# Kernel optimization log

Hardware: AMD Instinct MI355X
Metric: run time of the kernel (lower is better)

## Reference

```python
import jax, jax.numpy as jnp
import numpy as np

# Config: 2 base samples x 3 views, 128x128 feature map, d_model=128, 8x8 window grid
D = 128; H = 128; W = 128; NS = 8; NV = 3; BV = 2
B = BV * NV            # batched views (queries concatenated along batch)
M = NV - 1             # kv views per query view
WH = H // NS; WW = W // NS; WSZ = WH * WW
SH = WH // 2; SW = WW // 2  # shift sizes


def _split_np(f, ns):  # channel-last split_feature, numpy (for mask gen)
    b, h, w, c = f.shape
    return f.reshape(b, ns, h // ns, ns, w // ns, c).transpose(0, 1, 3, 2, 4, 5).reshape(b * ns * ns, h // ns, w // ns, c)


def _make_mask():  # generate_shift_window_attn_mask, structurally identical
    img = np.zeros((1, H, W, 1), np.float32)
    h_sl = [(0, H - WH), (H - WH, H - SH), (H - SH, H)]
    w_sl = [(0, W - WW), (W - WW, W - SW), (W - SW, W)]
    cnt = 0
    for h0, h1 in h_sl:
        for w0, w1 in w_sl:
            img[:, h0:h1, w0:w1, :] = cnt
            cnt += 1
    mw = _split_np(img, NS).reshape(-1, WSZ)               # [num_windows, WSZ]
    am = mw[:, None, :] - mw[:, :, None]
    return np.where(am != 0, np.float32(-100.0), np.float32(0.0))


def setup_inputs() -> dict:
    key = jax.random.key(0)
    ks = jax.random.split(key, 12)
    s = 1.0 / np.sqrt(D)
    s2 = 1.0 / np.sqrt(2 * D)
    s8 = 1.0 / np.sqrt(8 * D)
    f32 = jnp.float32
    inp = {
        'source': jax.random.normal(ks[0], (B, H * W, D), f32),
        'kv': jax.random.normal(ks[1], (B, M, H * W, D), f32),
        'attn_mask': jnp.asarray(_make_mask()),
        # self-attn layer (no ffn)
        'q1_w': jax.random.normal(ks[2], (D, D), f32) * s,
        'k1_w': jax.random.normal(ks[3], (D, D), f32) * s,
        'v1_w': jax.random.normal(ks[4], (D, D), f32) * s,
        'merge1_w': jax.random.normal(ks[5], (D, D), f32) * s,
        'ln1_g': jnp.ones((D,), f32), 'ln1_b': jnp.zeros((D,), f32),
        # cross-attn + ffn layer
        'q2_w': jax.random.normal(ks[6], (D, D), f32) * s,
        'k2_w': jax.random.normal(ks[7], (D, D), f32) * s,
        'v2_w': jax.random.normal(ks[8], (D, D), f32) * s,
        'merge2_w': jax.random.normal(ks[9], (D, D), f32) * s,
        'ln2a_g': jnp.ones((D,), f32), 'ln2a_b': jnp.zeros((D,), f32),
        'mlp_w1': jax.random.normal(ks[10], (2 * D, 8 * D), f32) * s2,
        'mlp_w2': jax.random.normal(ks[11], (8 * D, D), f32) * s8,
        'ln2b_g': jnp.ones((D,), f32), 'ln2b_b': jnp.zeros((D,), f32),
        'height': H, 'width': W, 'num_splits': NS,
    }
    return inp


def _split(x, ns):  # channel-last split_feature
    b, h, w, c = x.shape
    return x.reshape(b, ns, h // ns, ns, w // ns, c).transpose(0, 1, 3, 2, 4, 5).reshape(b * ns * ns, h // ns, w // ns, c)


def _merge(x, ns):  # channel-last merge_splits
    b, h, w, c = x.shape
    nb = b // (ns * ns)
    return x.reshape(nb, ns, ns, h, w, c).transpose(0, 1, 3, 2, 4, 5).reshape(nb, ns * h, ns * w, c)


def _ln(x, g, b):
    mu = x.mean(-1, keepdims=True)
    v = ((x - mu) ** 2).mean(-1, keepdims=True)
    return (x - mu) / jnp.sqrt(v + 1e-5) * g + b


def _self_win_attn(q, k, v, mask, h, w, ns):  # 3-dim path, with_shift=True
    b, _, c = q.shape
    sh, sw = (h // ns) // 2, (w // ns) // 2
    q = jnp.roll(q.reshape(b, h, w, c), (-sh, -sw), (1, 2))
    k = jnp.roll(k.reshape(b, h, w, c), (-sh, -sw), (1, 2))
    v = jnp.roll(v.reshape(b, h, w, c), (-sh, -sw), (1, 2))
    bn = b * ns * ns
    qf = _split(q, ns).reshape(bn, -1, c)
    kf = _split(k, ns).reshape(bn, -1, c)
    vf = _split(v, ns).reshape(bn, -1, c)
    sc = jnp.einsum('bqc,bkc->bqk', qf, kf) / (c ** 0.5) + jnp.tile(mask, (b, 1, 1))
    out = jax.nn.softmax(sc, -1) @ vf
    out = _merge(out.reshape(bn, h // ns, w // ns, c), ns)
    out = jnp.roll(out, (sh, sw), (1, 2))
    return out.reshape(b, -1, c)


def _cross_win_attn(q, k, v, mask, h, w, ns):  # 4-dim path (multi-view kv), with_shift=True
    b, _, c = q.shape
    m = k.shape[1]
    sh, sw = (h // ns) // 2, (w // ns) // 2
    q = jnp.roll(q.reshape(b, h, w, c), (-sh, -sw), (1, 2))
    k = jnp.roll(k.reshape(b, m, h, w, c), (-sh, -sw), (2, 3))
    v = jnp.roll(v.reshape(b, m, h, w, c), (-sh, -sw), (2, 3))
    bn = b * ns * ns
    wh, ww = h // ns, w // ns
    qf = _split(q, ns).reshape(bn, -1, c)
    kf = _split(jnp.transpose(k, (0, 2, 3, 4, 1)).reshape(b, h, w, c * m), ns)
    vf = _split(jnp.transpose(v, (0, 2, 3, 4, 1)).reshape(b, h, w, c * m), ns)
    kmat = jnp.transpose(kf.reshape(bn, wh, ww, c, m), (0, 3, 1, 2, 4)).reshape(bn, c, -1)  # [bn,c,WSZ*m]
    vmat = jnp.transpose(vf.reshape(bn, wh, ww, c, m), (0, 1, 2, 4, 3)).reshape(bn, -1, c)  # [bn,WSZ*m,c]
    sc = jnp.einsum('bqc,bck->bqk', qf, kmat) / (c ** 0.5) + jnp.tile(mask, (b, 1, m))
    out = jax.nn.softmax(sc, -1) @ vmat
    out = _merge(out.reshape(bn, wh, ww, c), ns)
    out = jnp.roll(out, (sh, sw), (1, 2))
    return out.reshape(b, -1, c)


def reference(source, kv, attn_mask, q1_w, k1_w, v1_w, merge1_w, ln1_g, ln1_b,
              q2_w, k2_w, v2_w, merge2_w, ln2a_g, ln2a_b, mlp_w1, mlp_w2, ln2b_g, ln2b_b,
              height, width, num_splits):
    h, w, ns = int(height), int(width), int(num_splits)
    # self-attention TransformerLayer (no_ffn=True)
    msg = _self_win_attn(source @ q1_w, source @ k1_w, source @ v1_w, attn_mask, h, w, ns)
    msg = _ln(msg @ merge1_w, ln1_g, ln1_b)
    src = source + msg
    # cross-attention TransformerLayer with FFN
    msg = _cross_win_attn(src @ q2_w, kv @ k2_w, kv @ v2_w, attn_mask, h, w, ns)
    msg = _ln(msg @ merge2_w, ln2a_g, ln2a_b)
    hid = jnp.concatenate([src, msg], -1) @ mlp_w1
    msg = _ln(jax.nn.gelu(hid, approximate=False) @ mlp_w2, ln2b_g, ln2b_b)
    return src + msg
```

## Files before the change

kernel.cpp:

```cpp
#include <hip/hip_runtime.h>
#include <math.h>


typedef float f4 __attribute__((ext_vector_type(4)));
typedef float f2 __attribute__((ext_vector_type(2)));
typedef float f32x4 __attribute__((ext_vector_type(4)));
typedef short s16x8 __attribute__((ext_vector_type(8)));
typedef short s16x4 __attribute__((ext_vector_type(4)));
typedef unsigned short u16;

constexpr int Dm   = 128;
constexpr int IH   = 128, IW = 128;
constexpr int Bq   = 6;
constexpr int Mv   = 2;
constexpr int WSZ  = 256;
constexpr int TOK  = IH * IW;
constexpr int ROWS = Bq * TOK;
constexpr int KVROWS = Bq * Mv * TOK;
constexpr int BN   = Bq * 64;
constexpr float SCALE = 0.08838834764831845f;

__device__ __forceinline__ u16 f2bf(float x) {
  union { float f; unsigned u; } v; v.f = x;
  unsigned r = v.u + 0x7fffu + ((v.u >> 16) & 1u);
  return (u16)(r >> 16);
}
__device__ __forceinline__ float bf2f(u16 h) {
  union { float f; unsigned u; } v; v.u = ((unsigned)h) << 16;
  return v.f;
}

__device__ __forceinline__ int dest_row_self(int r) {
  int b = r >> 14;
  int p = r & 16383;
  int y = p >> 7, x = p & 127;
  int Y = (y + 120) & 127, X = (x + 120) & 127;
  int bn = (b << 6) + ((Y >> 4) << 3) + (X >> 4);
  int t  = ((Y & 15) << 4) + (X & 15);
  return bn * WSZ + t;
}

__device__ __forceinline__ int dest_row_cross(int r) {
  int b  = r >> 15;
  int vi = (r >> 14) & 1;
  int p  = r & 16383;
  int y = p >> 7, x = p & 127;
  int Y = (y + 120) & 127, X = (x + 120) & 127;
  int bn = (b << 6) + ((Y >> 4) << 3) + (X >> 4);
  int t  = ((Y & 15) << 4) + (X & 15);
  return bn * (WSZ * Mv) + t * Mv + vi;
}

template<int NMAT, int MODE>
__global__ __launch_bounds__(256, 2)
void proj_kernel(const float* __restrict__ A,
                 const float* __restrict__ B0, const float* __restrict__ B1,
                 const float* __restrict__ B2,
                 float* __restrict__ O0, float* __restrict__ O1,
                 float* __restrict__ O2)
{
  __shared__ float At[128][68];
  __shared__ float Bs[64][132];
  const int tid  = threadIdx.x;
  const int row0 = blockIdx.x * 64;

  {
    const int tr = tid >> 2;
    const int tc = (tid & 3) * 4;
    const float* Ar = A + (size_t)(row0 + tr) * Dm;
    #pragma unroll
    for (int i = 0; i < 8; ++i) {
      int c = tc + i * 16;
      f4 a = *(const f4*)(Ar + c);
      At[c + 0][tr] = a[0];
      At[c + 1][tr] = a[1];
      At[c + 2][tr] = a[2];
      At[c + 3][tr] = a[3];
    }
  }

  const int tcol = tid & 31;
  const int trow = tid >> 5;

  int drow[8];
  #pragma unroll
  for (int i = 0; i < 8; ++i) {
    int r = row0 + trow * 8 + i;
    drow[i] = (MODE == 2) ? dest_row_cross(r) : dest_row_self(r);
  }

  #pragma unroll
  for (int m = 0; m < NMAT; ++m) {
    const float* Bm = (m == 0) ? B0 : ((m == 1) ? B1 : B2);
    float*       Om = (m == 0) ? O0 : ((m == 1) ? O1 : O2);
    float acc[8][4];
    #pragma unroll
    for (int i = 0; i < 8; ++i)
      #pragma unroll
      for (int j = 0; j < 4; ++j) acc[i][j] = 0.f;

    for (int kc = 0; kc < 2; ++kc) {
      __syncthreads();
      {
        int kb = tid >> 2;
        int cb = (tid & 3) * 4;
        #pragma unroll
        for (int i = 0; i < 8; ++i) {
          int c = cb + i * 16;
          f4 b = *(const f4*)(Bm + (size_t)(kc * 64 + kb) * Dm + c);
          *(f4*)&Bs[kb][c] = b;
        }
      }
      __syncthreads();
      #pragma unroll 4
      for (int k = 0; k < 64; ++k) {
        int kg = kc * 64 + k;
        f4 a0 = *(const f4*)&At[kg][trow * 8];
        f4 a1 = *(const f4*)&At[kg][trow * 8 + 4];
        f4 b  = *(const f4*)&Bs[k][tcol * 4];
        #pragma unroll
        for (int j = 0; j < 4; ++j) {
          acc[0][j] += a0[0] * b[j];
          acc[1][j] += a0[1] * b[j];
          acc[2][j] += a0[2] * b[j];
          acc[3][j] += a0[3] * b[j];
          acc[4][j] += a1[0] * b[j];
          acc[5][j] += a1[1] * b[j];
          acc[6][j] += a1[2] * b[j];
          acc[7][j] += a1[3] * b[j];
        }
      }
    }
    #pragma unroll
    for (int i = 0; i < 8; ++i) {
      f4 o;
      o[0] = acc[i][0]; o[1] = acc[i][1]; o[2] = acc[i][2]; o[3] = acc[i][3];
      *(f4*)(Om + (size_t)drow[i] * Dm + tcol * 4) = o;
    }
  }
}

template<int MM>
__global__ __launch_bounds__(512, 2)
void attn_kernel(const float* __restrict__ Qw, const float* __restrict__ Kw,
                 const float* __restrict__ Vw, float* __restrict__ X)
{
  constexpr int KC = WSZ * MM;
  __shared__ float Qt[128][36];
  __shared__ float Stg[128 * 132];
  __shared__ float S[32][KC + 1];

  const int tid = threadIdx.x;
  const int bn  = blockIdx.y;
  const int q0  = blockIdx.x * 32;
  const int b   = bn >> 6;
  const int win = bn & 63;
  const int wy  = win >> 3, wx = win & 7;

  {
    const float* Qbase = Qw + ((size_t)bn * WSZ + q0) * Dm;
    #pragma unroll
    for (int j = 0; j < 2; ++j) {
      int id  = tid + j * 512;
      int row = id >> 5;
      int c   = (id & 31) * 4;
      f4 a = *(const f4*)(Qbase + row * Dm + c);
      Qt[c + 0][row] = a[0]; Qt[c + 1][row] = a[1];
      Qt[c + 2][row] = a[2]; Qt[c + 3][row] = a[3];
    }
  }

  auto region = [&](int t) -> int {
    int rh = (wy == 7) ? (((t >> 4) >= 8) ? 2 : 1) : 0;
    int rw = (wx == 7) ? (((t & 15) >= 8) ? 2 : 1) : 0;
    return rh * 3 + rw;
  };

  const int kg = tid & 31;
  const int qg = tid >> 5;
  const int rq0 = region(q0 + qg * 2);
  const int rq1 = region(q0 + qg * 2 + 1);

  for (int ch = 0; ch < KC / 128; ++ch) {
    __syncthreads();
    #pragma unroll
    for (int j = 0; j < 8; ++j) {
      int id  = tid + j * 512;
      int key = id >> 5;
      int c   = (id & 31) * 4;
      f4 kvv = *(const f4*)(Kw + ((size_t)bn * KC + ch * 128 + key) * Dm + c);
      Stg[(c + 0) * 132 + key] = kvv[0];
      Stg[(c + 1) * 132 + key] = kvv[1];
      Stg[(c + 2) * 132 + key] = kvv[2];
      Stg[(c + 3) * 132 + key] = kvv[3];
    }
    __syncthreads();
    float a00 = 0, a01 = 0, a02 = 0, a03 = 0;
    float a10 = 0, a11 = 0, a12 = 0, a13 = 0;
    #pragma unroll 4
    for (int c = 0; c < 128; ++c) {
      f2 qv  = *(const f2*)&Qt[c][qg * 2];
      f4 kv4 = *(const f4*)&Stg[c * 132 + kg * 4];
      a00 += qv[0] * kv4[0]; a01 += qv[0] * kv4[1];
      a02 += qv[0] * kv4[2]; a03 += qv[0] * kv4[3];
      a10 += qv[1] * kv4[0]; a11 += qv[1] * kv4[1];
      a12 += qv[1] * kv4[2]; a13 += qv[1] * kv4[3];
    }
    float s0[4] = {a00, a01, a02, a03};
    float s1[4] = {a10, a11, a12, a13};
    #pragma unroll
    for (int j = 0; j < 4; ++j) {
      int kk = ch * 128 + kg * 4 + j;
      int rk = region(kk & 255);
      S[qg * 2 + 0][kk] = s0[j] * SCALE + ((rq0 == rk) ? 0.f : -100.f);
      S[qg * 2 + 1][kk] = s1[j] * SCALE + ((rq1 == rk) ? 0.f : -100.f);
    }
  }
  __syncthreads();

  {
    int row = tid >> 4, l = tid & 15;
    float mx = -1e30f;
    for (int k = l; k < KC; k += 16) mx = fmaxf(mx, S[row][k]);
    #pragma unroll
    for (int msk = 1; msk < 16; msk <<= 1) mx = fmaxf(mx, __shfl_xor(mx, msk));
    float sum = 0.f;
    for (int k = l; k < KC; k += 16) {
      float e = expf(S[row][k] - mx);
      S[row][k] = e;
      sum += e;
    }
    #pragma unroll
    for (int msk = 1; msk < 16; msk <<= 1) sum += __shfl_xor(sum, msk);
    float inv = 1.0f / sum;
    for (int k = l; k < KC; k += 16) S[row][k] *= inv;
  }

  const int cg = tid & 31;
  const int rg = tid >> 5;
  float o00 = 0, o01 = 0, o02 = 0, o03 = 0;
  float o10 = 0, o11 = 0, o12 = 0, o13 = 0;
  for (int ch = 0; ch < KC / 128; ++ch) {
    __syncthreads();
    #pragma unroll
    for (int j = 0; j < 8; ++j) {
      int id  = tid + j * 512;
      int key = id >> 5;
      int c   = (id & 31) * 4;
      f4 vv = *(const f4*)(Vw + ((size_t)bn * KC + ch * 128 + key) * Dm + c);
      *(f4*)&Stg[key * 132 + c] = vv;
    }
    __syncthreads();
    #pragma unroll 4
    for (int k = 0; k < 128; ++k) {
      int kk = ch * 128 + k;
      float p0 = S[rg * 2 + 0][kk];
      float p1 = S[rg * 2 + 1][kk];
      f4 vv = *(const f4*)&Stg[k * 132 + cg * 4];
      o00 += p0 * vv[0]; o01 += p0 * vv[1]; o02 += p0 * vv[2]; o03 += p0 * vv[3];
      o10 += p1 * vv[0]; o11 += p1 * vv[1]; o12 += p1 * vv[2]; o13 += p1 * vv[3];
    }
  }
  #pragma unroll
  for (int i = 0; i < 2; ++i) {
    int t  = q0 + rg * 2 + i;
    int iy = t >> 4, ix = t & 15;
    int y = (wy * 16 + iy + 8) & 127;
    int x = (wx * 16 + ix + 8) & 127;
    f4 o;
    if (i == 0) { o[0] = o00; o[1] = o01; o[2] = o02; o[3] = o03; }
    else        { o[0] = o10; o[1] = o11; o[2] = o12; o[3] = o13; }
    *(f4*)(X + ((size_t)(b * TOK + y * IW + x)) * Dm + cg * 4) = o;
  }
}

template<bool ADD>
__global__ __launch_bounds__(256, 2)
void merge_ln_kernel(const float* __restrict__ Xin, const float* __restrict__ Wm,
                     const float* __restrict__ g, const float* __restrict__ bi,
                     const float* __restrict__ srcAdd, float* __restrict__ Out)
{
  __shared__ float At[128][68];
  __shared__ float Bs[64][132];
  const int tid  = threadIdx.x;
  const int row0 = blockIdx.x * 64;

  {
    const int tr = tid >> 2;
    const int tc = (tid & 3) * 4;
    const float* Ar = Xin + (size_t)(row0 + tr) * Dm;
    #pragma unroll
    for (int i = 0; i < 8; ++i) {
      int c = tc + i * 16;
      f4 a = *(const f4*)(Ar + c);
      At[c + 0][tr] = a[0]; At[c + 1][tr] = a[1];
      At[c + 2][tr] = a[2]; At[c + 3][tr] = a[3];
    }
  }

  const int tcol = tid & 31;
  const int trow = tid >> 5;
  float acc[8][4];
  #pragma unroll
  for (int i = 0; i < 8; ++i)
    #pragma unroll
    for (int j = 0; j < 4; ++j) acc[i][j] = 0.f;

  for (int kc = 0; kc < 2; ++kc) {
    __syncthreads();
    {
      int kb = tid >> 2;
      int cb = (tid & 3) * 4;
      #pragma unroll
      for (int i = 0; i < 8; ++i) {
        int c = cb + i * 16;
        f4 b = *(const f4*)(Wm + (size_t)(kc * 64 + kb) * Dm + c);
        *(f4*)&Bs[kb][c] = b;
      }
    }
    __syncthreads();
    #pragma unroll 4
    for (int k = 0; k < 64; ++k) {
      int kg = kc * 64 + k;
      f4 a0 = *(const f4*)&At[kg][trow * 8];
      f4 a1 = *(const f4*)&At[kg][trow * 8 + 4];
      f4 b  = *(const f4*)&Bs[k][tcol * 4];
      #pragma unroll
      for (int j = 0; j < 4; ++j) {
        acc[0][j] += a0[0] * b[j];
        acc[1][j] += a0[1] * b[j];
        acc[2][j] += a0[2] * b[j];
        acc[3][j] += a0[3] * b[j];
        acc[4][j] += a1[0] * b[j];
        acc[5][j] += a1[1] * b[j];
        acc[6][j] += a1[2] * b[j];
        acc[7][j] += a1[3] * b[j];
      }
    }
  }

  f4 g4 = *(const f4*)(g + tcol * 4);
  f4 b4 = *(const f4*)(bi + tcol * 4);
  #pragma unroll
  for (int i = 0; i < 8; ++i) {
    float s = acc[i][0] + acc[i][1] + acc[i][2] + acc[i][3];
    #pragma unroll
    for (int msk = 1; msk < 32; msk <<= 1) s += __shfl_xor(s, msk);
    float mu = s * (1.0f / 128.0f);
    float d0 = acc[i][0] - mu, d1 = acc[i][1] - mu;
    float d2 = acc[i][2] - mu, d3 = acc[i][3] - mu;
    float qs = d0 * d0 + d1 * d1 + d2 * d2 + d3 * d3;
    #pragma unroll
    for (int msk = 1; msk < 32; msk <<= 1) qs += __shfl_xor(qs, msk);
    float rstd = 1.0f / sqrtf(qs * (1.0f / 128.0f) + 1e-5f);
    int r = row0 + trow * 8 + i;
    f4 o;
    o[0] = d0 * rstd * g4[0] + b4[0];
    o[1] = d1 * rstd * g4[1] + b4[1];
    o[2] = d2 * rstd * g4[2] + b4[2];
    o[3] = d3 * rstd * g4[3] + b4[3];
    if (ADD) {
      f4 sv = *(const f4*)(srcAdd + (size_t)r * Dm + tcol * 4);
      o += sv;
    }
    *(f4*)(Out + (size_t)r * Dm + tcol * 4) = o;
  }
}

__global__ __launch_bounds__(256)
void prep_weights(const float* __restrict__ W1, const float* __restrict__ W2,
                  u16* __restrict__ w1h, u16* __restrict__ w1l,
                  u16* __restrict__ w2h, u16* __restrict__ w2l)
{
  int id = blockIdx.x * 256 + threadIdx.x;
  if (id < 262144) {
    int i  = id & 7;
    int ln = (id >> 3) & 63;
    int ks = (id >> 9) & 7;
    int ct = (id >> 12) & 7;
    int c  = id >> 15;
    int k   = ks * 32 + (ln >> 4) * 8 + i;
    int col = c * 128 + ct * 16 + (ln & 15);
    float v = W1[(size_t)k * 1024 + col];
    u16 h = f2bf(v);
    w1h[id] = h;
    w1l[id] = f2bf(v - bf2f(h));
  } else {
    int id2 = id - 262144;
    int i  = id2 & 7;
    int ln = (id2 >> 3) & 63;
    int ct = (id2 >> 9) & 7;
    int ks = (id2 >> 12) & 3;
    int c  = id2 >> 14;
    int k   = c * 128 + ks * 32 + (ln >> 4) * 8 + i;
    int col = ct * 16 + (ln & 15);
    float v = W2[(size_t)k * 128 + col];
    u16 h = f2bf(v);
    w2h[id2] = h;
    w2l[id2] = f2bf(v - bf2f(h));
  }
}

__global__ __launch_bounds__(512)
void mlp_mfma_kernel(const float* __restrict__ SRC, const float* __restrict__ MSG,
                     const u16* __restrict__ w1h, const u16* __restrict__ w1l,
                     const u16* __restrict__ w2h, const u16* __restrict__ w2l,
                     const float* __restrict__ g, const float* __restrict__ bi,
                     float* __restrict__ Out)
{
  __shared__ __align__(16) u16 Xh[64 * 256];
  __shared__ __align__(16) u16 Xl[64 * 256];
  __shared__ __align__(16) u16 Hh[64 * 128];
  __shared__ __align__(16) u16 Hl[64 * 128];

  const int tid  = threadIdx.x;
  const int row0 = blockIdx.x * 64;
  const int l    = tid & 63;
  const int w    = tid >> 6;
  const int rt   = w & 3;
  const int ctg  = w >> 2;

  #pragma unroll
  for (int s = 0; s < 8; ++s) {
    int slot = tid + s * 512;
    int row  = slot >> 6;
    int c4   = (slot & 63) * 4;
    const float* p = (c4 < 128) ? (SRC + (size_t)(row0 + row) * Dm + c4)
                                : (MSG + (size_t)(row0 + row) * Dm + (c4 - 128));
    f4 a = *(const f4*)p;
    s16x4 hv, lv;
    #pragma unroll
    for (int i = 0; i < 4; ++i) {
// ... 110 lines not shown
      int cc = sub * 4 + s * 32;
      f4 g4 = *(const f4*)(g + cc);
      f4 b4 = *(const f4*)(bi + cc);
      f4 rv = *(const f4*)(SRC + (size_t)(row0 + row) * Dm + cc);
      f4 o = v[s] * rstd * g4 + b4 + rv;
      *(f4*)(Out + (size_t)(row0 + row) * Dm + cc) = o;
    }
  }
}

extern "C" void kernel_launch(void* const* d_in, const int* in_sizes, int n_in,
                              void* d_out, int out_size, void* d_ws, size_t ws_size,
                              hipStream_t stream)
{
  const float* source = (const float*)d_in[0];
  const float* kv     = (const float*)d_in[1];
  const float* q1    = (const float*)d_in[3];
  const float* k1    = (const float*)d_in[4];
  const float* v1    = (const float*)d_in[5];
  const float* m1    = (const float*)d_in[6];
  const float* ln1g  = (const float*)d_in[7];
  const float* ln1b  = (const float*)d_in[8];
  const float* q2    = (const float*)d_in[9];
  const float* k2    = (const float*)d_in[10];
  const float* v2    = (const float*)d_in[11];
  const float* m2    = (const float*)d_in[12];
  const float* ln2ag = (const float*)d_in[13];
  const float* ln2ab = (const float*)d_in[14];
  const float* w1    = (const float*)d_in[15];
  const float* w2    = (const float*)d_in[16];
  const float* ln2bg = (const float*)d_in[17];
  const float* ln2bb = (const float*)d_in[18];

  float* ws   = (float*)d_ws;
  float* Qw   = ws;
  float* Kw   = Qw + (size_t)BN * WSZ * Dm;
  float* Vw   = Kw + (size_t)BN * WSZ * Mv * Dm;
  float* SRCb = Vw + (size_t)BN * WSZ * Mv * Dm;
  float* MSG2 = Qw;
  float* X    = (float*)d_out;

  u16* w1h = (u16*)Vw;
  u16* w1l = w1h + 262144;
  u16* w2h = w1l + 262144;
  u16* w2l = w2h + 131072;

  proj_kernel<3, 0><<<ROWS / 64, 256, 0, stream>>>(source, q1, k1, v1, Qw, Kw, Vw);
  attn_kernel<1><<<dim3(8, BN), 512, 0, stream>>>(Qw, Kw, Vw, X);
  merge_ln_kernel<true><<<ROWS / 64, 256, 0, stream>>>(X, m1, ln1g, ln1b, source, SRCb);
  proj_kernel<1, 1><<<ROWS / 64, 256, 0, stream>>>(SRCb, q2, nullptr, nullptr,
                                                   Qw, nullptr, nullptr);
  proj_kernel<2, 2><<<KVROWS / 64, 256, 0, stream>>>(kv, k2, v2, nullptr,
                                                     Kw, Vw, nullptr);
  attn_kernel<2><<<dim3(8, BN), 512, 0, stream>>>(Qw, Kw, Vw, X);
  merge_ln_kernel<false><<<ROWS / 64, 256, 0, stream>>>(X, m2, ln2ag, ln2ab,
                                                        nullptr, MSG2);
  prep_weights<<<1536, 256, 0, stream>>>(w1, w2, w1h, w1l, w2h, w2l);
  mlp_mfma_kernel<<<ROWS / 64, 512, 0, stream>>>(SRCb, MSG2, w1h, w1l, w2h, w2l,
                                                 ln2bg, ln2bb, (float*)d_out);
}
```

Baseline: 2.455 ms.

## Move projections, window attention and merge to split-bf16 MFMA kernels

Replaces the scalar fp32 projection, attention and merge+LayerNorm kernels with MFMA versions that split each operand into bf16 high/low parts (three products per tile) to stay close to fp32 accuracy. Attention becomes a flash-style online softmax over 64-key chunks with a transposed V layout, and projections gather rows from window order rather than scattering outputs. Weight fragments are prepared by small prep kernels, and the workspace buffers are laid out again to hold the hi/lo arrays. The aim is to move the dominant FLOPs onto matrix cores, at the cost of triple MFMA work and more intermediate memory traffic for the hi/lo bf16 copies.

```diff
diff --git a/kernel.cpp b/kernel.cpp
--- a/kernel.cpp
+++ b/kernel.cpp
@@ -3,20 +3,17 @@
 
 
 typedef float f4 __attribute__((ext_vector_type(4)));
-typedef float f2 __attribute__((ext_vector_type(2)));
 typedef float f32x4 __attribute__((ext_vector_type(4)));
 typedef short s16x8 __attribute__((ext_vector_type(8)));
 typedef short s16x4 __attribute__((ext_vector_type(4)));
 typedef unsigned short u16;
 
 constexpr int Dm   = 128;
-constexpr int IH   = 128, IW = 128;
 constexpr int Bq   = 6;
 constexpr int Mv   = 2;
 constexpr int WSZ  = 256;
-constexpr int TOK  = IH * IW;
+constexpr int TOK  = 16384;
 constexpr int ROWS = Bq * TOK;
-constexpr int KVROWS = Bq * Mv * TOK;
 constexpr int BN   = Bq * 64;
 constexpr float SCALE = 0.08838834764831845f;
 
@@ -30,374 +27,463 @@
   return v.f;
 }
 
-__device__ __forceinline__ int dest_row_self(int r) {
-  int b = r >> 14;
-  int p = r & 16383;
-  int y = p >> 7, x = p & 127;
-  int Y = (y + 120) & 127, X = (x + 120) & 127;
-  int bn = (b << 6) + ((Y >> 4) << 3) + (X >> 4);
-  int t  = ((Y & 15) << 4) + (X & 15);
-  return bn * WSZ + t;
-}
-
-__device__ __forceinline__ int dest_row_cross(int r) {
-  int b  = r >> 15;
-  int vi = (r >> 14) & 1;
-  int p  = r & 16383;
-  int y = p >> 7, x = p & 127;
-  int Y = (y + 120) & 127, X = (x + 120) & 127;
-  int bn = (b << 6) + ((Y >> 4) << 3) + (X >> 4);
-  int t  = ((Y & 15) << 4) + (X & 15);
-  return bn * (WSZ * Mv) + t * Mv + vi;
-}
-
-template<int NMAT, int MODE>
-__global__ __launch_bounds__(256, 2)
-void proj_kernel(const float* __restrict__ A,
-                 const float* __restrict__ B0, const float* __restrict__ B1,
-                 const float* __restrict__ B2,
-                 float* __restrict__ O0, float* __restrict__ O1,
-                 float* __restrict__ O2)
+__global__ __launch_bounds__(256)
+void prep_dxd(const float* __restrict__ W0, const float* __restrict__ W1,
+              const float* __restrict__ W2, u16* __restrict__ dst)
 {
-  __shared__ float At[128][68];
-  __shared__ float Bs[64][132];
-  const int tid  = threadIdx.x;
-  const int row0 = blockIdx.x * 64;
-
-  {
-    const int tr = tid >> 2;
-    const int tc = (tid & 3) * 4;
-    const float* Ar = A + (size_t)(row0 + tr) * Dm;
-    #pragma unroll
-    for (int i = 0; i < 8; ++i) {
-      int c = tc + i * 16;
-      f4 a = *(const f4*)(Ar + c);
-      At[c + 0][tr] = a[0];
-      At[c + 1][tr] = a[1];
-      At[c + 2][tr] = a[2];
-      At[c + 3][tr] = a[3];
-    }
-  }
-
-  const int tcol = tid & 31;
-  const int trow = tid >> 5;
-
-  int drow[8];
-  #pragma unroll
-  for (int i = 0; i < 8; ++i) {
-    int r = row0 + trow * 8 + i;
-    drow[i] = (MODE == 2) ? dest_row_cross(r) : dest_row_self(r);
-  }
-
-  #pragma unroll
-  for (int m = 0; m < NMAT; ++m) {
-    const float* Bm = (m == 0) ? B0 : ((m == 1) ? B1 : B2);
-    float*       Om = (m == 0) ? O0 : ((m == 1) ? O1 : O2);
-    float acc[8][4];
-    #pragma unroll
-    for (int i = 0; i < 8; ++i)
-      #pragma unroll
-      for (int j = 0; j < 4; ++j) acc[i][j] = 0.f;
-
-    for (int kc = 0; kc < 2; ++kc) {
-      __syncthreads();
-      {
-        int kb = tid >> 2;
-        int cb = (tid & 3) * 4;
-        #pragma unroll
-        for (int i = 0; i < 8; ++i) {
-          int c = cb + i * 16;
-          f4 b = *(const f4*)(Bm + (size_t)(kc * 64 + kb) * Dm + c);
-          *(f4*)&Bs[kb][c] = b;
-        }
-      }
-      __syncthreads();
-      #pragma unroll 4
-      for (int k = 0; k < 64; ++k) {
-        int kg = kc * 64 + k;
-        f4 a0 = *(const f4*)&At[kg][trow * 8];
-        f4 a1 = *(const f4*)&At[kg][trow * 8 + 4];
-        f4 b  = *(const f4*)&Bs[k][tcol * 4];
-        #pragma unroll
-        for (int j = 0; j < 4; ++j) {
-          acc[0][j] += a0[0] * b[j];
-          acc[1][j] += a0[1] * b[j];
-          acc[2][j] += a0[2] * b[j];
-          acc[3][j] += a0[3] * b[j];
-          acc[4][j] += a1[0] * b[j];
-          acc[5][j] += a1[1] * b[j];
-          acc[6][j] += a1[2] * b[j];
-          acc[7][j] += a1[3] * b[j];
-        }
-      }
-    }
-    #pragma unroll
-    for (int i = 0; i < 8; ++i) {
-      f4 o;
-      o[0] = acc[i][0]; o[1] = acc[i][1]; o[2] = acc[i][2]; o[3] = acc[i][3];
-      *(f4*)(Om + (size_t)drow[i] * Dm + tcol * 4) = o;
-    }
-  }
-}
-
-template<int MM>
-__global__ __launch_bounds__(512, 2)
-void attn_kernel(const float* __restrict__ Qw, const float* __restrict__ Kw,
-                 const float* __restrict__ Vw, float* __restrict__ X)
-{
-  constexpr int KC = WSZ * MM;
-  __shared__ float Qt[128][36];
-  __shared__ float Stg[128 * 132];
-  __shared__ float S[32][KC + 1];
-
-  const int tid = threadIdx.x;
-  const int bn  = blockIdx.y;
-  const int q0  = blockIdx.x * 32;
-  const int b   = bn >> 6;
-  const int win = bn & 63;
-  const int wy  = win >> 3, wx = win & 7;
-
-  {
-    const float* Qbase = Qw + ((size_t)bn * WSZ + q0) * Dm;
-    #pragma unroll
-    for (int j = 0; j < 2; ++j) {
-      int id  = tid + j * 512;
-      int row = id >> 5;
-      int c   = (id & 31) * 4;
-      f4 a = *(const f4*)(Qbase + row * Dm + c);
-      Qt[c + 0][row] = a[0]; Qt[c + 1][row] = a[1];
-      Qt[c + 2][row] = a[2]; Qt[c + 3][row] = a[3];
-    }
-  }
-
-  auto region = [&](int t) -> int {
-    int rh = (wy == 7) ? (((t >> 4) >= 8) ? 2 : 1) : 0;
-    int rw = (wx == 7) ? (((t & 15) >= 8) ? 2 : 1) : 0;
-    return rh * 3 + rw;
-  };
-
-  const int kg = tid & 31;
-  const int qg = tid >> 5;
-  const int rq0 = region(q0 + qg * 2);
-  const int rq1 = region(q0 + qg * 2 + 1);
-
-  for (int ch = 0; ch < KC / 128; ++ch) {
-    __syncthreads();
-    #pragma unroll
-    for (int j = 0; j < 8; ++j) {
-      int id  = tid + j * 512;
-      int key = id >> 5;
-      int c   = (id & 31) * 4;
-      f4 kvv = *(const f4*)(Kw + ((size_t)bn * KC + ch * 128 + key) * Dm + c);
-      Stg[(c + 0) * 132 + key] = kvv[0];
-      Stg[(c + 1) * 132 + key] = kvv[1];
-      Stg[(c + 2) * 132 + key] = kvv[2];
-      Stg[(c + 3) * 132 + key] = kvv[3];
-    }
-    __syncthreads();
-    float a00 = 0, a01 = 0, a02 = 0, a03 = 0;
-    float a10 = 0, a11 = 0, a12 = 0, a13 = 0;
-    #pragma unroll 4
-    for (int c = 0; c < 128; ++c) {
-      f2 qv  = *(const f2*)&Qt[c][qg * 2];
-      f4 kv4 = *(const f4*)&Stg[c * 132 + kg * 4];
-      a00 += qv[0] * kv4[0]; a01 += qv[0] * kv4[1];
-      a02 += qv[0] * kv4[2]; a03 += qv[0] * kv4[3];
-      a10 += qv[1] * kv4[0]; a11 += qv[1] * kv4[1];
-      a12 += qv[1] * kv4[2]; a13 += qv[1] * kv4[3];
-    }
-    float s0[4] = {a00, a01, a02, a03};
-    float s1[4] = {a10, a11, a12, a13};
-    #pragma unroll
-    for (int j = 0; j < 4; ++j) {
-      int kk = ch * 128 + kg * 4 + j;
-      int rk = region(kk & 255);
-      S[qg * 2 + 0][kk] = s0[j] * SCALE + ((rq0 == rk) ? 0.f : -100.f);
-      S[qg * 2 + 1][kk] = s1[j] * SCALE + ((rq1 == rk) ? 0.f : -100.f);
-    }
-  }
-  __syncthreads();
-
-  {
-    int row = tid >> 4, l = tid & 15;
-    float mx = -1e30f;
-    for (int k = l; k < KC; k += 16) mx = fmaxf(mx, S[row][k]);
-    #pragma unroll
-    for (int msk = 1; msk < 16; msk <<= 1) mx = fmaxf(mx, __shfl_xor(mx, msk));
-    float sum = 0.f;
-    for (int k = l; k < KC; k += 16) {
-      float e = expf(S[row][k] - mx);
-      S[row][k] = e;
-      sum += e;
-    }
-    #pragma unroll
-    for (int msk = 1; msk < 16; msk <<= 1) sum += __shfl_xor(sum, msk);
-    float inv = 1.0f / sum;
-    for (int k = l; k < KC; k += 16) S[row][k] *= inv;
-  }
-
-  const int cg = tid & 31;
-  const int rg = tid >> 5;
-  float o00 = 0, o01 = 0, o02 = 0, o03 = 0;
-  float o10 = 0, o11 = 0, o12 = 0, o13 = 0;
-  for (int ch = 0; ch < KC / 128; ++ch) {
-    __syncthreads();
-    #pragma unroll
-    for (int j = 0; j < 8; ++j) {
-      int id  = tid + j * 512;
-      int key = id >> 5;
-      int c   = (id & 31) * 4;
-      f4 vv = *(const f4*)(Vw + ((size_t)bn * KC + ch * 128 + key) * Dm + c);
-      *(f4*)&Stg[key * 132 + c] = vv;
-    }
-    __syncthreads();
-    #pragma unroll 4
-    for (int k = 0; k < 128; ++k) {
-      int kk = ch * 128 + k;
-      float p0 = S[rg * 2 + 0][kk];
-      float p1 = S[rg * 2 + 1][kk];
-      f4 vv = *(const f4*)&Stg[k * 132 + cg * 4];
-      o00 += p0 * vv[0]; o01 += p0 * vv[1]; o02 += p0 * vv[2]; o03 += p0 * vv[3];
-      o10 += p1 * vv[0]; o11 += p1 * vv[1]; o12 += p1 * vv[2]; o13 += p1 * vv[3];
-    }
-  }
-  #pragma unroll
-  for (int i = 0; i < 2; ++i) {
-    int t  = q0 + rg * 2 + i;
-    int iy = t >> 4, ix = t & 15;
-    int y = (wy * 16 + iy + 8) & 127;
-    int x = (wx * 16 + ix + 8) & 127;
-    f4 o;
-    if (i == 0) { o[0] = o00; o[1] = o01; o[2] = o02; o[3] = o03; }
-    else        { o[0] = o10; o[1] = o11; o[2] = o12; o[3] = o13; }
-    *(f4*)(X + ((size_t)(b * TOK + y * IW + x)) * Dm + cg * 4) = o;
-  }
-}
-
-template<bool ADD>
-__global__ __launch_bounds__(256, 2)
-void merge_ln_kernel(const float* __restrict__ Xin, const float* __restrict__ Wm,
-                     const float* __restrict__ g, const float* __restrict__ bi,
-                     const float* __restrict__ srcAdd, float* __restrict__ Out)
-{
-  __shared__ float At[128][68];
-  __shared__ float Bs[64][132];
-  const int tid  = threadIdx.x;
-  const int row0 = blockIdx.x * 64;
-
-  {
-    const int tr = tid >> 2;
-    const int tc = (tid & 3) * 4;
-    const float* Ar = Xin + (size_t)(row0 + tr) * Dm;
-    #pragma unroll
-    for (int i = 0; i < 8; ++i) {
-      int c = tc + i * 16;
-      f4 a = *(const f4*)(Ar + c);
-      At[c + 0][tr] = a[0]; At[c + 1][tr] = a[1];
-      At[c + 2][tr] = a[2]; At[c + 3][tr] = a[3];
-    }
-  }
-
-  const int tcol = tid & 31;
-  const int trow = tid >> 5;
-  float acc[8][4];
-  #pragma unroll
-  for (int i = 0; i < 8; ++i)
-    #pragma unroll
-    for (int j = 0; j < 4; ++j) acc[i][j] = 0.f;
-
-  for (int kc = 0; kc < 2; ++kc) {
-    __syncthreads();
-    {
-      int kb = tid >> 2;
-      int cb = (tid & 3) * 4;
-      #pragma unroll
-      for (int i = 0; i < 8; ++i) {
-        int c = cb + i * 16;
-        f4 b = *(const f4*)(Wm + (size_t)(kc * 64 + kb) * Dm + c);
-        *(f4*)&Bs[kb][c] = b;
-      }
-    }
-    __syncthreads();
-    #pragma unroll 4
-    for (int k = 0; k < 64; ++k) {
-      int kg = kc * 64 + k;
-      f4 a0 = *(const f4*)&At[kg][trow * 8];
-      f4 a1 = *(const f4*)&At[kg][trow * 8 + 4];
-      f4 b  = *(const f4*)&Bs[k][tcol * 4];
-      #pragma unroll
-      for (int j = 0; j < 4; ++j) {
-        acc[0][j] += a0[0] * b[j];
-        acc[1][j] += a0[1] * b[j];
-        acc[2][j] += a0[2] * b[j];
-        acc[3][j] += a0[3] * b[j];
-        acc[4][j] += a1[0] * b[j];
-        acc[5][j] += a1[1] * b[j];
-        acc[6][j] += a1[2] * b[j];
-        acc[7][j] += a1[3] * b[j];
-      }
-    }
-  }
-
-  f4 g4 = *(const f4*)(g + tcol * 4);
-  f4 b4 = *(const f4*)(bi + tcol * 4);
-  #pragma unroll
-  for (int i = 0; i < 8; ++i) {
-    float s = acc[i][0] + acc[i][1] + acc[i][2] + acc[i][3];
-    #pragma unroll
-    for (int msk = 1; msk < 32; msk <<= 1) s += __shfl_xor(s, msk);
-    float mu = s * (1.0f / 128.0f);
-    float d0 = acc[i][0] - mu, d1 = acc[i][1] - mu;
-    float d2 = acc[i][2] - mu, d3 = acc[i][3] - mu;
-    float qs = d0 * d0 + d1 * d1 + d2 * d2 + d3 * d3;
-    #pragma unroll
-    for (int msk = 1; msk < 32; msk <<= 1) qs += __shfl_xor(qs, msk);
-    float rstd = 1.0f / sqrtf(qs * (1.0f / 128.0f) + 1e-5f);
-    int r = row0 + trow * 8 + i;
-    f4 o;
-    o[0] = d0 * rstd * g4[0] + b4[0];
-    o[1] = d1 * rstd * g4[1] + b4[1];
-    o[2] = d2 * rstd * g4[2] + b4[2];
-    o[3] = d3 * rstd * g4[3] + b4[3];
-    if (ADD) {
-      f4 sv = *(const f4*)(srcAdd + (size_t)r * Dm + tcol * 4);
-      o += sv;
-    }
-    *(f4*)(Out + (size_t)r * Dm + tcol * 4) = o;
-  }
+  int gid = blockIdx.x * 256 + threadIdx.x;
+  int widx = gid >> 14;
+  int id = gid & 16383;
+  const float* W = (widx == 0) ? W0 : ((widx == 1) ? W1 : W2);
+  int i = id & 7, ln = (id >> 3) & 63, ks = (id >> 9) & 3, ct = id >> 11;
+  int k = ks * 32 + (ln >> 4) * 8 + i;
+  int col = ct * 16 + (ln & 15);
+  float v = W[k * 128 + col];
+  u16 h = f2bf(v);
+  u16* wp = dst + widx * 32768;
+  wp[id] = h;
+  wp[16384 + id] = f2bf(v - bf2f(h));
 }
 
 __global__ __launch_bounds__(256)
-void prep_weights(const float* __restrict__ W1, const float* __restrict__ W2,
-                  u16* __restrict__ w1h, u16* __restrict__ w1l,
-                  u16* __restrict__ w2h, u16* __restrict__ w2l)
+void prep_w1w2m2(const float* __restrict__ W1, const float* __restrict__ W2,
+                 const float* __restrict__ M2,
+                 u16* __restrict__ w1h, u16* __restrict__ w1l,
+                 u16* __restrict__ w2h, u16* __restrict__ w2l,
+                 u16* __restrict__ m2h, u16* __restrict__ m2l)
 {
   int id = blockIdx.x * 256 + threadIdx.x;
   if (id < 262144) {
-    int i  = id & 7;
-    int ln = (id >> 3) & 63;
-    int ks = (id >> 9) & 7;
-    int ct = (id >> 12) & 7;
-    int c  = id >> 15;
-    int k   = ks * 32 + (ln >> 4) * 8 + i;
+    int i = id & 7, ln = (id >> 3) & 63, ks = (id >> 9) & 7;
+    int ct = (id >> 12) & 7, c = id >> 15;
+    int k = ks * 32 + (ln >> 4) * 8 + i;
     int col = c * 128 + ct * 16 + (ln & 15);
     float v = W1[(size_t)k * 1024 + col];
     u16 h = f2bf(v);
-    w1h[id] = h;
-    w1l[id] = f2bf(v - bf2f(h));
-  } else {
+    w1h[id] = h; w1l[id] = f2bf(v - bf2f(h));
+  } else if (id < 393216) {
     int id2 = id - 262144;
-    int i  = id2 & 7;
-    int ln = (id2 >> 3) & 63;
-    int ct = (id2 >> 9) & 7;
-    int ks = (id2 >> 12) & 3;
-    int c  = id2 >> 14;
-    int k   = c * 128 + ks * 32 + (ln >> 4) * 8 + i;
+    int i = id2 & 7, ln = (id2 >> 3) & 63, ct = (id2 >> 9) & 7;
+    int ks = (id2 >> 12) & 3, c = id2 >> 14;
+    int k = c * 128 + ks * 32 + (ln >> 4) * 8 + i;
     int col = ct * 16 + (ln & 15);
     float v = W2[(size_t)k * 128 + col];
     u16 h = f2bf(v);
-    w2h[id2] = h;
-    w2l[id2] = f2bf(v - bf2f(h));
+    w2h[id2] = h; w2l[id2] = f2bf(v - bf2f(h));
+  } else {
+    int id3 = id - 393216;
+    int i = id3 & 7, ln = (id3 >> 3) & 63, ks = (id3 >> 9) & 3, ct = id3 >> 11;
+    int k = ks * 32 + (ln >> 4) * 8 + i;
+    int col = ct * 16 + (ln & 15);
+    float v = M2[k * 128 + col];
+    u16 h = f2bf(v);
+    m2h[id3] = h; m2l[id3] = f2bf(v - bf2f(h));
+  }
+}
+
+template<int MODE, int NMAT, int KC>
+__global__ __launch_bounds__(256, 2)
+void proj_mfma(const float* __restrict__ A,
+               const u16* __restrict__ wh0, const u16* __restrict__ wl0,
+               const u16* __restrict__ wh1, const u16* __restrict__ wl1,
+               const u16* __restrict__ wh2, const u16* __restrict__ wl2,
+               u16* __restrict__ q_h, u16* __restrict__ q_l,
+               u16* __restrict__ k_h, u16* __restrict__ k_l,
+               u16* __restrict__ v_h, u16* __restrict__ v_l)
+{
+  __shared__ __align__(16) u16 Ah[64 * 128];
+  __shared__ __align__(16) u16 Al[64 * 128];
+  __shared__ __align__(16) float ob[64 * 132];
+  const int tid = threadIdx.x;
+  const int l = tid & 63, w = tid >> 6;
+  const int row0 = blockIdx.x * 64;
+
+  #pragma unroll
+  for (int it = 0; it < 8; ++it) {
+    int task = tid + it * 256;
+    int r = task >> 5, c4 = (task & 31) * 4;
+    int rw = row0 + r;
+    int src;
+    if (MODE == 2) {
+      int bn = rw >> 9, bb = bn >> 6, win = bn & 63, kk = rw & 511;
+      int t = kk >> 1, vi = kk & 1;
+      int y = (((win >> 3) << 4) + (t >> 4) + 8) & 127;
+      int x = (((win & 7) << 4) + (t & 15) + 8) & 127;
+      src = ((bb * 2 + vi) << 14) + (y << 7) + x;
+    } else {
+      int bn = rw >> 8, bb = bn >> 6, win = bn & 63, t = rw & 255;
+      int y = (((win >> 3) << 4) + (t >> 4) + 8) & 127;
+      int x = (((win & 7) << 4) + (t & 15) + 8) & 127;
+      src = (bb << 14) + (y << 7) + x;
+    }
+    f4 a = *(const f4*)(A + (size_t)src * Dm + c4);
+    s16x4 hv, lv;
+    #pragma unroll
+    for (int i = 0; i < 4; ++i) {
+      u16 h = f2bf(a[i]);
+      hv[i] = (short)h;
+      lv[i] = (short)f2bf(a[i] - bf2f(h));
+    }
+    int word = r * 64 + ((c4 >> 1) ^ ((r & 7) << 2));
+    *(s16x4*)&Ah[word * 2] = hv;
+    *(s16x4*)&Al[word * 2] = lv;
+  }
+  __syncthreads();
+
+  const int awb = (w * 16 + (l & 15)) * 64;
+  const int swz = (l & 7) << 2;
+  const int kg4 = (l >> 4) * 4;
+
+  #pragma unroll
+  for (int m = 0; m < NMAT; ++m) {
+    const u16* bhp = (m == 0) ? wh0 : ((m == 1) ? wh1 : wh2);
+    const u16* blp = (m == 0) ? wl0 : ((m == 1) ? wl1 : wl2);
+    f32x4 acc[8];
+    #pragma unroll
+    for (int i = 0; i < 8; ++i) acc[i] = (f32x4)(0.f);
+    #pragma unroll
+    for (int ks = 0; ks < 4; ++ks) {
+      int word = awb + ((ks * 16 + kg4) ^ swz);
+      s16x8 ah = *(const s16x8*)&Ah[word * 2];
+      s16x8 al = *(const s16x8*)&Al[word * 2];
+      #pragma unroll
+      for (int ct = 0; ct < 8; ++ct) {
+        size_t fo = (size_t)(((ct * 4 + ks) * 64) + l) * 8;
+        s16x8 bh = *(const s16x8*)(bhp + fo);
+        s16x8 bl = *(const s16x8*)(blp + fo);
+        acc[ct] = __builtin_amdgcn_mfma_f32_16x16x32_bf16(ah, bh, acc[ct], 0, 0, 0);
+        acc[ct] = __builtin_amdgcn_mfma_f32_16x16x32_bf16(ah, bl, acc[ct], 0, 0, 0);
+        acc[ct] = __builtin_amdgcn_mfma_f32_16x16x32_bf16(al, bh, acc[ct], 0, 0, 0);
+      }
+    }
+    __syncthreads();
+    #pragma unroll
+    for (int ct = 0; ct < 8; ++ct)
+      #pragma unroll
+      for (int j = 0; j < 4; ++j)
+        ob[(w * 16 + (l >> 4) * 4 + j) * 132 + ct * 16 + (l & 15)] = acc[ct][j];
+    __syncthreads();
+
+    const bool isVt = (MODE == 0 && m == 2) || (MODE == 2 && m == 1);
+    if (!isVt) {
+      u16* oh = (m == 0) ? q_h : k_h;
+      u16* ol = (m == 0) ? q_l : k_l;
+      #pragma unroll
+      for (int it = 0; it < 4; ++it) {
+        int task = tid + it * 256;
+        int r = task >> 4, h0 = (task & 15) * 8;
+        f4 x0 = *(const f4*)&ob[r * 132 + h0];
+        f4 x1 = *(const f4*)&ob[r * 132 + h0 + 4];
+        s16x8 hv, lv;
+        #pragma unroll
+        for (int i = 0; i < 4; ++i) {
+          u16 h = f2bf(x0[i]); hv[i] = (short)h; lv[i] = (short)f2bf(x0[i] - bf2f(h));
+          u16 h2 = f2bf(x1[i]); hv[4 + i] = (short)h2; lv[4 + i] = (short)f2bf(x1[i] - bf2f(h2));
+        }
+        *(s16x8*)(oh + (size_t)(row0 + r) * Dm + h0) = hv;
+        *(s16x8*)(ol + (size_t)(row0 + r) * Dm + h0) = lv;
+      }
+    } else {
+      const int bn = row0 >> ((MODE == 2) ? 9 : 8);
+      const int kk0 = row0 & (KC - 1);
+      #pragma unroll
+      for (int it = 0; it < 4; ++it) {
+        int task = tid + it * 256;
+        int d = task >> 3, k0 = (task & 7) * 8;
+        s16x8 hv, lv;
+        #pragma unroll
+        for (int i = 0; i < 8; ++i) {
+          float vv = ob[(k0 + i) * 132 + d];
+          u16 h = f2bf(vv); hv[i] = (short)h; lv[i] = (short)f2bf(vv - bf2f(h));
+        }
+        size_t off = ((size_t)bn * 128 + d) * KC + kk0 + k0;
+        *(s16x8*)(v_h + off) = hv;
+        *(s16x8*)(v_l + off) = lv;
+      }
+    }
+  }
+}
+
+template<bool ADD>
+__global__ __launch_bounds__(256, 2)
+void merge_mfma(const float* __restrict__ Xin,
+                const u16* __restrict__ wh, const u16* __restrict__ wl,
+                const float* __restrict__ g, const float* __restrict__ bi,
+                const float* __restrict__ resid, float* __restrict__ Out)
+{
+  __shared__ __align__(16) u16 Ah[64 * 128];
+  __shared__ __align__(16) u16 Al[64 * 128];
+  __shared__ __align__(16) float ob[64 * 132];
+  __shared__ float mus[64], rsts[64];
+  const int tid = threadIdx.x;
+  const int l = tid & 63, w = tid >> 6;
+  const int row0 = blockIdx.x * 64;
+
+  #pragma unroll
+  for (int it = 0; it < 8; ++it) {
+    int task = tid + it * 256;
+    int r = task >> 5, c4 = (task & 31) * 4;
+    f4 a = *(const f4*)(Xin + (size_t)(row0 + r) * Dm + c4);
+    s16x4 hv, lv;
+    #pragma unroll
+    for (int i = 0; i < 4; ++i) {
+      u16 h = f2bf(a[i]);
+      hv[i] = (short)h;
+      lv[i] = (short)f2bf(a[i] - bf2f(h));
+    }
+    int word = r * 64 + ((c4 >> 1) ^ ((r & 7) << 2));
+    *(s16x4*)&Ah[word * 2] = hv;
+    *(s16x4*)&Al[word * 2] = lv;
+  }
+  __syncthreads();
+
+  const int awb = (w * 16 + (l & 15)) * 64;
+  const int swz = (l & 7) << 2;
+  const int kg4 = (l >> 4) * 4;
+
+  f32x4 acc[8];
+  #pragma unroll
+  for (int i = 0; i < 8; ++i) acc[i] = (f32x4)(0.f);
+  #pragma unroll
+  for (int ks = 0; ks < 4; ++ks) {
+    int word = awb + ((ks * 16 + kg4) ^ swz);
+    s16x8 ah = *(const s16x8*)&Ah[word * 2];
+    s16x8 al = *(const s16x8*)&Al[word * 2];
+    #pragma unroll
+    for (int ct = 0; ct < 8; ++ct) {
+      size_t fo = (size_t)(((ct * 4 + ks) * 64) + l) * 8;
+      s16x8 bh = *(const s16x8*)(wh + fo);
+      s16x8 bl = *(const s16x8*)(wl + fo);
+      acc[ct] = __builtin_amdgcn_mfma_f32_16x16x32_bf16(ah, bh, acc[ct], 0, 0, 0);
+      acc[ct] = __builtin_amdgcn_mfma_f32_16x16x32_bf16(ah, bl, acc[ct], 0, 0, 0);
+      acc[ct] = __builtin_amdgcn_mfma_f32_16x16x32_bf16(al, bh, acc[ct], 0, 0, 0);
+    }
+  }
+
+  float s[4] = {0.f, 0.f, 0.f, 0.f}, qq[4] = {0.f, 0.f, 0.f, 0.f};
+  #pragma unroll
+  for (int ct = 0; ct < 8; ++ct)
+    #pragma unroll
+    for (int j = 0; j < 4; ++j) {
+      float v = acc[ct][j];
+      s[j] += v; qq[j] += v * v;
+    }
+  #pragma unroll
+  for (int j = 0; j < 4; ++j) {
+    s[j] += __shfl_xor(s[j], 1); s[j] += __shfl_xor(s[j], 2);
+    s[j] += __shfl_xor(s[j], 4); s[j] += __shfl_xor(s[j], 8);
+    qq[j] += __shfl_xor(qq[j], 1); qq[j] += __shfl_xor(qq[j], 2);
+    qq[j] += __shfl_xor(qq[j], 4); qq[j] += __shfl_xor(qq[j], 8);
+  }
+  if ((l & 15) == 0) {
+    #pragma unroll
+    for (int j = 0; j < 4; ++j) {
+      int r = w * 16 + (l >> 4) * 4 + j;
+      float mu = s[j] * (1.0f / 128.0f);
+      float var = qq[j] * (1.0f / 128.0f) - mu * mu;
+      mus[r] = mu;
+      rsts[r] = 1.0f / sqrtf(var + 1e-5f);
+    }
+  }
+  #pragma unroll
+  for (int ct = 0; ct < 8; ++ct)
+    #pragma unroll
+    for (int j = 0; j < 4; ++j)
+      ob[(w * 16 + (l >> 4) * 4 + j) * 132 + ct * 16 + (l & 15)] = acc[ct][j];
+  __syncthreads();
+
+  #pragma unroll
+  for (int it = 0; it < 8; ++it) {
+    int task = tid + it * 256;
+    int r = task >> 5, c4 = (task & 31) * 4;
+    f4 v = *(const f4*)&ob[r * 132 + c4];
+    float mu = mus[r], rs = rsts[r];
+    f4 g4 = *(const f4*)(g + c4);
+    f4 b4 = *(const f4*)(bi + c4);
+    f4 o = (v - mu) * rs * g4 + b4;
+    if (ADD) o += *(const f4*)(resid + (size_t)(row0 + r) * Dm + c4);
+    *(f4*)(Out + (size_t)(row0 + r) * Dm + c4) = o;
+  }
+}
+
+template<int MM>
+__global__ __launch_bounds__(512, 2)
+void attn_mfma(const u16* __restrict__ Qh, const u16* __restrict__ Ql,
+               const u16* __restrict__ Kh, const u16* __restrict__ Kl,
+               const u16* __restrict__ Vth, const u16* __restrict__ Vtl,
+               float* __restrict__ X)
+{
+  constexpr int KC = 256 * MM;
+  constexpr int NCH = KC / 64;
+  __shared__ __align__(16) u16 lds[65536];
+  u16* Khs = lds;
+  u16* Kls = lds + 8192;
+  u16* Vhs = lds + 16384;
+  u16* Vls = lds + 24576;
+  const int tid = threadIdx.x, l = tid & 63, w = tid >> 6;
+  u16* Phs = lds + 32768 + w * 2048;
+  u16* Pls = lds + 49152 + w * 2048;
+
+  const int bn = blockIdx.x, b = bn >> 6, win = bn & 63;
+  const int wy = win >> 3, wx = win & 7;
+
+  s16x8 qfh[2][4], qfl[2][4];
+  #pragma unroll
+  for (int qt = 0; qt < 2; ++qt)
+    #pragma unroll
+    for (int ks = 0; ks < 4; ++ks) {
+      size_t off = ((size_t)bn * WSZ + w * 32 + qt * 16 + (l & 15)) * Dm
+                 + ks * 32 + (l >> 4) * 8;
+      qfh[qt][ks] = *(const s16x8*)(Qh + off);
+      qfl[qt][ks] = *(const s16x8*)(Ql + off);
+    }
+
+  auto region = [&](int t) -> int {
+    int rh = (wy == 7) ? (((t >> 4) >= 8) ? 2 : 1) : 0;
+    int rw_ = (wx == 7) ? (((t & 15) >= 8) ? 2 : 1) : 0;
+    return rh * 3 + rw_;
+  };
+  int rq[2][4];
+  #pragma unroll
+  for (int qt = 0; qt < 2; ++qt)
+    #pragma unroll
+    for (int j = 0; j < 4; ++j)
+      rq[qt][j] = region(w * 32 + qt * 16 + (l >> 4) * 4 + j);
+
+  f32x4 o[2][8];
+  #pragma unroll
+  for (int qt = 0; qt < 2; ++qt)
+    #pragma unroll
+    for (int dt = 0; dt < 8; ++dt) o[qt][dt] = (f32x4)(0.f);
+  float mrow[2][4], lrow[2][4];
+  #pragma unroll
+  for (int qt = 0; qt < 2; ++qt)
+    #pragma unroll
+    for (int j = 0; j < 4; ++j) { mrow[qt][j] = -1e30f; lrow[qt][j] = 0.f; }
+
+  const int swz2 = (l & 7) << 2;
+  const int swz3 = (l & 7) << 3;
+
+  for (int ch = 0; ch < NCH; ++ch) {
+    __syncthreads();
+    #pragma unroll
+    for (int it = 0; it < 2; ++it) {
+      int task = tid + it * 512;
+      int r = task >> 4, hc = (task & 15) * 8;
+      size_t src = ((size_t)bn * KC + ch * 64 + r) * Dm + hc;
+      int word = r * 64 + ((hc >> 1) ^ ((r & 7) << 2));
+      *(s16x8*)&Khs[word * 2] = *(const s16x8*)(Kh + src);
+      *(s16x8*)&Kls[word * 2] = *(const s16x8*)(Kl + src);
+    }
+    #pragma unroll
+    for (int it = 0; it < 2; ++it) {
+      int task = tid + it * 512;
+      int d = task >> 3, hc = (task & 7) * 8;
+      size_t src = ((size_t)bn * 128 + d) * KC + ch * 64 + hc;
+      int word = d * 32 + ((hc >> 1) ^ ((d & 7) << 2));
+      *(s16x8*)&Vhs[word * 2] = *(const s16x8*)(Vth + src);
+      *(s16x8*)&Vls[word * 2] = *(const s16x8*)(Vtl + src);
+    }
+    __syncthreads();
+
+    #pragma unroll
+    for (int qt = 0; qt < 2; ++qt) {
+      float pb[4][4];
+      #pragma unroll
+      for (int kt = 0; kt < 4; ++kt) {
+        f32x4 sc = (f32x4)(0.f);
+        #pragma unroll
+        for (int ks = 0; ks < 4; ++ks) {
+          int word = (kt * 16 + (l & 15)) * 64 + ((ks * 16 + (l >> 4) * 4) ^ swz2);
+          s16x8 bh = *(const s16x8*)&Khs[word * 2];
+          s16x8 bl = *(const s16x8*)&Kls[word * 2];
+          sc = __builtin_amdgcn_mfma_f32_16x16x32_bf16(qfh[qt][ks], bh, sc, 0, 0, 0);
+          sc = __builtin_amdgcn_mfma_f32_16x16x32_bf16(qfh[qt][ks], bl, sc, 0, 0, 0);
+          sc = __builtin_amdgcn_mfma_f32_16x16x32_bf16(qfl[qt][ks], bh, sc, 0, 0, 0);
+        }
+        int kk = ch * 64 + kt * 16 + (l & 15);
+        int rk = region(kk & 255);
+        #pragma unroll
+        for (int j = 0; j < 4; ++j)
+          pb[kt][j] = sc[j] * SCALE + ((rq[qt][j] == rk) ? 0.f : -100.f);
+      }
+      #pragma unroll
+      for (int j = 0; j < 4; ++j) {
+        float pm = fmaxf(fmaxf(pb[0][j], pb[1][j]), fmaxf(pb[2][j], pb[3][j]));
+        pm = fmaxf(pm, __shfl_xor(pm, 1));
+        pm = fmaxf(pm, __shfl_xor(pm, 2));
+        pm = fmaxf(pm, __shfl_xor(pm, 4));
+        pm = fmaxf(pm, __shfl_xor(pm, 8));
+        float mold = mrow[qt][j];
+        float mnew = fmaxf(mold, pm);
+        float f = __expf(mold - mnew);
+        mrow[qt][j] = mnew;
+        lrow[qt][j] *= f;
+        #pragma unroll
+        for (int dt = 0; dt < 8; ++dt) o[qt][dt][j] *= f;
+        int qloc = qt * 16 + (l >> 4) * 4 + j;
+        int sw = (qloc & 7) << 3;
+        #pragma unroll
+        for (int kt = 0; kt < 4; ++kt) {
+          float p = __expf(pb[kt][j] - mnew);
+          lrow[qt][j] += p;
+          u16 ph = f2bf(p);
+          u16 pl = f2bf(p - bf2f(ph));
+          int key = kt * 16 + (l & 15);
+          int hidx = qloc * 64 + (key ^ sw);
+          Phs[hidx] = ph;
+          Pls[hidx] = pl;
+        }
+      }
+    }
+
+    #pragma unroll
+    for (int qt = 0; qt < 2; ++qt)
+      #pragma unroll
+      for (int ks2 = 0; ks2 < 2; ++ks2) {
+        int hidxA = (qt * 16 + (l & 15)) * 64 + ((ks2 * 32 + (l >> 4) * 8) ^ swz3);
+        s16x8 ah = *(const s16x8*)&Phs[hidxA];
+        s16x8 al = *(const s16x8*)&Pls[hidxA];
+        #pragma unroll
+        for (int dt = 0; dt < 8; ++dt) {
+          int word = (dt * 16 + (l & 15)) * 32 + ((ks2 * 16 + (l >> 4) * 4) ^ swz2);
+          s16x8 bh = *(const s16x8*)&Vhs[word * 2];
+          s16x8 bl = *(const s16x8*)&Vls[word * 2];
+          o[qt][dt] = __builtin_amdgcn_mfma_f32_16x16x32_bf16(ah, bh, o[qt][dt], 0, 0, 0);
+          o[qt][dt] = __builtin_amdgcn_mfma_f32_16x16x32_bf16(ah, bl, o[qt][dt], 0, 0, 0);
+          o[qt][dt] = __builtin_amdgcn_mfma_f32_16x16x32_bf16(al, bh, o[qt][dt], 0, 0, 0);
+        }
+      }
+  }
+
+  float linv[2][4];
+  #pragma unroll
+  for (int qt = 0; qt < 2; ++qt)
+    #pragma unroll
+    for (int j = 0; j < 4; ++j) {
+      float sv = lrow[qt][j];
+      sv += __shfl_xor(sv, 1); sv += __shfl_xor(sv, 2);
+      sv += __shfl_xor(sv, 4); sv += __shfl_xor(sv, 8);
+      linv[qt][j] = 1.0f / sv;
+    }
+  __syncthreads();
+  float* ob = (float*)lds;
+  #pragma unroll
+  for (int qt = 0; qt < 2; ++qt)
+    #pragma unroll
+    for (int dt = 0; dt < 8; ++dt)
+      #pragma unroll
+      for (int j = 0; j < 4; ++j)
+        ob[(w * 32 + qt * 16 + (l >> 4) * 4 + j) * 128 + dt * 16 + (l & 15)] =
+            o[qt][dt][j] * linv[qt][j];
+  __syncthreads();
+  #pragma unroll
+  for (int it = 0; it < 16; ++it) {
+    int task = tid + it * 512;
+    int r = task >> 5, c4 = (task & 31) * 4;
+    int y = ((wy << 4) + (r >> 4) + 8) & 127;
+    int x = ((wx << 4) + (r & 15) + 8) & 127;
+    *(f4*)(X + ((size_t)(b << 14) + (y << 7) + x) * Dm + c4) = *(const f4*)&ob[r * 128 + c4];
   }
 }
 
@@ -574,30 +660,53 @@
   const float* ln2bg = (const float*)d_in[17];
   const float* ln2bb = (const float*)d_in[18];
 
-  float* ws   = (float*)d_ws;
-  float* Qw   = ws;
-  float* Kw   = Qw + (size_t)BN * WSZ * Dm;
-  float* Vw   = Kw + (size_t)BN * WSZ * Mv * Dm;
-  float* SRCb = Vw + (size_t)BN * WSZ * Mv * Dm;
-  float* MSG2 = Qw;
-  float* X    = (float*)d_out;
-
-  u16* w1h = (u16*)Vw;
+  char* base = (char*)d_ws;
+  char* Ab = base;
+  char* Bb = base + 50331648;
+  char* Cb = Bb + 100663296;
+  char* Db = Cb + 100663296;
+
+  u16* Qh = (u16*)Ab;
+  u16* Ql = (u16*)(Ab + 25165824);
+  float* MSG2 = (float*)Ab;
+  u16* Kh = (u16*)Bb;
+  u16* Kl_s = (u16*)(Bb + 25165824);
+  u16* Kl_c = (u16*)(Bb + 50331648);
+  u16* Vth = (u16*)Cb;
+  u16* Vtl_s = (u16*)(Cb + 25165824);
+  u16* Vtl_c = (u16*)(Cb + 50331648);
+  float* X = (float*)Db;
+  float* SRCb = (float*)d_out;
+
+  u16* fragD  = (u16*)Db;
+  u16* fragB2 = (u16*)(Bb + 50331648);
+  u16* w1h = (u16*)Bb;
   u16* w1l = w1h + 262144;
   u16* w2h = w1l + 262144;
   u16* w2l = w2h + 131072;
-
-  proj_kernel<3, 0><<<ROWS / 64, 256, 0, stream>>>(source, q1, k1, v1, Qw, Kw, Vw);
-  attn_kernel<1><<<dim3(8, BN), 512, 0, stream>>>(Qw, Kw, Vw, X);
-  merge_ln_kernel<true><<<ROWS / 64, 256, 0, stream>>>(X, m1, ln1g, ln1b, source, SRCb);
-  proj_kernel<1, 1><<<ROWS / 64, 256, 0, stream>>>(SRCb, q2, nullptr, nullptr,
-                                                   Qw, nullptr, nullptr);
-  proj_kernel<2, 2><<<KVROWS / 64, 256, 0, stream>>>(kv, k2, v2, nullptr,
-                                                     Kw, Vw, nullptr);
-  attn_kernel<2><<<dim3(8, BN), 512, 0, stream>>>(Qw, Kw, Vw, X);
-  merge_ln_kernel<false><<<ROWS / 64, 256, 0, stream>>>(X, m2, ln2ag, ln2ab,
-                                                        nullptr, MSG2);
-  prep_weights<<<1536, 256, 0, stream>>>(w1, w2, w1h, w1l, w2h, w2l);
-  mlp_mfma_kernel<<<ROWS / 64, 512, 0, stream>>>(SRCb, MSG2, w1h, w1l, w2h, w2l,
-                                                 ln2bg, ln2bb, (float*)d_out);
-}
+  u16* m2h = w2l + 131072;
+  u16* m2l = m2h + 16384;
+
+  prep_dxd<<<192, 256, 0, stream>>>(q1, k1, v1, fragD);
+  prep_dxd<<<128, 256, 0, stream>>>(m1, q2, q2, fragB2);
+  proj_mfma<0, 3, 256><<<1536, 256, 0, stream>>>(
+      source, fragD, fragD + 16384, fragD + 32768, fragD + 49152,
+      fragD + 65536, fragD + 81920,
+      Qh, Ql, Kh, Kl_s, Vth, Vtl_s);
+  attn_mfma<1><<<384, 512, 0, stream>>>(Qh, Ql, Kh, Kl_s, Vth, Vtl_s, X);
+  merge_mfma<true><<<1536, 256, 0, stream>>>(X, fragB2, fragB2 + 16384,
+                                             ln1g, ln1b, source, SRCb);
+  prep_dxd<<<128, 256, 0, stream>>>(k2, v2, v2, fragD);
+  proj_mfma<1, 1, 256><<<1536, 256, 0, stream>>>(
+      SRCb, fragB2 + 32768, fragB2 + 49152, nullptr, nullptr, nullptr, nullptr,
+      Qh, Ql, nullptr, nullptr, nullptr, nullptr);
+  proj_mfma<2, 2, 512><<<3072, 256, 0, stream>>>(
+      kv, fragD, fragD + 16384, fragD + 32768, fragD + 49152, nullptr, nullptr,
+      Kh, Kl_c, nullptr, nullptr, Vth, Vtl_c);
+  attn_mfma<2><<<384, 512, 0, stream>>>(Qh, Ql, Kh, Kl_c, Vth, Vtl_c, X);
+  prep_w1w2m2<<<1600, 256, 0, stream>>>(w1, w2, m2, w1h, w1l, w2h, w2l, m2h, m2l);
+  merge_mfma<false><<<1536, 256, 0, stream>>>(X, m2h, m2l, ln2ag, ln2ab,
+                                              nullptr, MSG2);
+  mlp_mfma_kernel<<<1536, 512, 0, stream>>>(SRCb, MSG2, w1h, w1l, w2h, w2l,
+                                            ln2bg, ln2bb, (float*)d_out);
+}
```

After: 2.102 ms. 14.4% less time.
